# Optimization experiments

Hardware: AMD Instinct MI355X
Metric: run time of the kernel (lower is better)

Reference implementation:

```python
import jax, jax.numpy as jnp
import numpy as np

NUM_USER, NUM_ITEM, NUM_TIME = 200000, 100000, 5000
P, Q, R = 32, 32, 32
N = 131072


def _xavier(key, shape):
    fan_in, fan_out = shape[0], int(np.prod(shape[1:]))
    limit = float(np.sqrt(6.0 / (fan_in + fan_out)))
    return jax.random.uniform(key, shape, dtype=jnp.float32, minval=-limit, maxval=limit)


def setup_inputs() -> dict:
    key = jax.random.key(0)
    k1, k2, k3, k4, k5, k6, k7 = jax.random.split(key, 7)
    return {
        "i_input": jax.random.randint(k1, (N,), 0, NUM_USER),
        "j_input": jax.random.randint(k2, (N,), 0, NUM_ITEM),
        "k_input": jax.random.randint(k3, (N,), 0, NUM_TIME),
        "user_embeddings": _xavier(k4, (NUM_USER, P)),
        "item_embeddings": _xavier(k5, (NUM_ITEM, Q)),
        "time_embeddings": _xavier(k6, (NUM_TIME, R)),
        "core_tensor": _xavier(k7, (P, Q, R)),
    }


def reference(i_input, j_input, k_input, user_embeddings, item_embeddings,
              time_embeddings, core_tensor):
    # Gather per-sample embeddings: [n,p], [n,q], [n,r]
    i_embeds = user_embeddings[i_input]
    j_embeds = item_embeddings[j_input]
    k_embeds = time_embeddings[k_input]
    # Fused Tucker contraction: never materialize the (n,p,q,r) outer product.
    # Mathematically identical to einsum('np,nq,nr,pqr->n', ...).
    t = jnp.einsum('np,pqr->nqr', i_embeds, core_tensor)  # [n,q,r]
    t = jnp.einsum('nqr,nq->nr', t, j_embeds)             # [n,r]
    return jnp.einsum('nr,nr->n', t, k_embeds)            # [n]
```

## Files before the change

### kernel.cpp

```cpp
#include <hip/hip_runtime.h>


#define BIN_CAP 128

__device__ __forceinline__ void build_H_body(const float* __restrict__ G,
                                             const float* __restrict__ W,
                                             float* __restrict__ H,
                                             int num_time, int bblk) {
    const int pq4 = threadIdx.x;
    const int kbase = bblk * 8;

    float acc[8][4];
#pragma unroll
    for (int kk = 0; kk < 8; ++kk)
#pragma unroll
        for (int i = 0; i < 4; ++i) acc[kk][i] = 0.f;

#pragma unroll
    for (int r4 = 0; r4 < 8; ++r4) {
        float4 g[4];
#pragma unroll
        for (int i = 0; i < 4; ++i)
            g[i] = *(const float4*)(G + (size_t)(pq4 * 4 + i) * 32 + r4 * 4);
#pragma unroll
        for (int kk = 0; kk < 8; ++kk) {
            int k = kbase + kk;
            int kc = (k < num_time) ? k : (num_time - 1);
            float4 w = *(const float4*)(W + (size_t)kc * 32 + r4 * 4);
#pragma unroll
            for (int i = 0; i < 4; ++i)
                acc[kk][i] += g[i].x * w.x + g[i].y * w.y + g[i].z * w.z + g[i].w * w.w;
        }
    }

#pragma unroll
    for (int kk = 0; kk < 8; ++kk) {
        int k = kbase + kk;
        if (k < num_time) {
            float4 o = make_float4(acc[kk][0], acc[kk][1], acc[kk][2], acc[kk][3]);
            *(float4*)(H + (size_t)k * 1024 + pq4 * 4) = o;
        }
    }
}

__device__ __forceinline__ void scatter_body(const int* __restrict__ K,
                                             const int* __restrict__ I,
                                             const int* __restrict__ J,
                                             int* __restrict__ counts,
                                             int4* __restrict__ bins,
                                             int* __restrict__ ovf_cnt,
                                             int4* __restrict__ ovf,
                                             int n, int sblk, int nsblk) {
    for (int idx = sblk * 256 + (int)threadIdx.x; idx < n; idx += nsblk * 256) {
        int k = K[idx];
        int4 rec = make_int4(idx, I[idx], J[idx], k);
        int pos = atomicAdd(&counts[k], 1);
        if (pos < BIN_CAP) {
            bins[(size_t)k * BIN_CAP + pos] = rec;
        } else {
            int o = atomicAdd(ovf_cnt, 1);
            ovf[o] = rec;
        }
    }
}

__global__ __launch_bounds__(256) void fused_prepare(
        const float* __restrict__ G, const float* __restrict__ W,
        float* __restrict__ H,
        const int* __restrict__ K, const int* __restrict__ I,
        const int* __restrict__ J, int* __restrict__ counts,
        int4* __restrict__ bins, int* __restrict__ ovf_cnt,
        int4* __restrict__ ovf, int n, int num_time,
        int nbuild, int nscatter) {
    const int b = blockIdx.x;
    if (b < nbuild) {
        build_H_body(G, W, H, num_time, b);
    } else {
        scatter_body(K, I, J, counts, bins, ovf_cnt, ovf, n, b - nbuild, nscatter);
    }
}

__global__ __launch_bounds__(256) void build_H(const float* __restrict__ G,
                                               const float* __restrict__ W,
                                               float* __restrict__ H,
                                               int num_time) {
    build_H_body(G, W, H, num_time, blockIdx.x);
}

__global__ __launch_bounds__(256) void tucker_eval_grouped(
        const float* __restrict__ U, const float* __restrict__ V,
        const float* __restrict__ H, const int* __restrict__ counts,
        const int4* __restrict__ bins, float* __restrict__ out,
        int num_time, const int* __restrict__ ovf_cnt,
        const int4* __restrict__ ovf) {
    __shared__ float4 Hs4[4][256];
    const int wave = threadIdx.x >> 6;
    const int lane = threadIdx.x & 63;
    const int k = blockIdx.x * 4 + wave;
    const int qq = lane & 7;
    const int s8 = lane >> 3;

    int m = 0;
    if (k < num_time) {
        const float4* __restrict__ Hrow4 = (const float4*)(H + (size_t)k * 1024);
#pragma unroll
        for (int c = 0; c < 4; ++c)
            Hs4[wave][lane + 64 * c] = Hrow4[lane + 64 * c];
        m = counts[k];
        m = (m < BIN_CAP) ? m : BIN_CAP;
    }
    __syncthreads();

    if (k < num_time && m > 0) {
        const int iters = (m + 7) >> 3;
        const float4* __restrict__ Hw = Hs4[wave];
        const int4* __restrict__ bbase = bins + (size_t)k * BIN_CAP;

        int sc = (s8 < m) ? s8 : (m - 1);
        int4 rec = bbase[sc];

        for (int t = 0; t < iters; ++t) {
            const int s = t * 8 + s8;
            const float4* __restrict__ Ur = (const float4*)(U + (size_t)rec.y * 32);
            float4 u[8];
#pragma unroll
            for (int p4 = 0; p4 < 8; ++p4) u[p4] = Ur[p4];
            float4 v4 = ((const float4*)(V + (size_t)rec.z * 32))[qq];

            int sn = s + 8;
            sn = (sn < m) ? sn : (m - 1);
            int4 rec_n = bbase[sn];

            float4 acc = make_float4(0.f, 0.f, 0.f, 0.f);
#pragma unroll
            for (int p4 = 0; p4 < 8; ++p4) {
                float4 h;
                h = Hw[(p4 * 4 + 0) * 8 + qq];
                acc.x += u[p4].x * h.x; acc.y += u[p4].x * h.y;
                acc.z += u[p4].x * h.z; acc.w += u[p4].x * h.w;
                h = Hw[(p4 * 4 + 1) * 8 + qq];
                acc.x += u[p4].y * h.x; acc.y += u[p4].y * h.y;
                acc.z += u[p4].y * h.z; acc.w += u[p4].y * h.w;
                h = Hw[(p4 * 4 + 2) * 8 + qq];
                acc.x += u[p4].z * h.x; acc.y += u[p4].z * h.y;
                acc.z += u[p4].z * h.z; acc.w += u[p4].z * h.w;
                h = Hw[(p4 * 4 + 3) * 8 + qq];
                acc.x += u[p4].w * h.x; acc.y += u[p4].w * h.y;
                acc.z += u[p4].w * h.z; acc.w += u[p4].w * h.w;
            }
            float sd = acc.x * v4.x + acc.y * v4.y + acc.z * v4.z + acc.w * v4.w;
            sd += __shfl_xor(sd, 1, 64);
            sd += __shfl_xor(sd, 2, 64);
            sd += __shfl_xor(sd, 4, 64);
            if (s < m && qq == 0) out[rec.x] = sd;
            rec = rec_n;
        }
    }

    const int cnt = *ovf_cnt;
    if (cnt > 0) {
        const int gwave = (int)blockIdx.x * 4 + wave;
        const int nw = (int)gridDim.x * 4;
        const int pg = lane >> 3;
        for (int s = gwave; s < cnt; s += nw) {
            int4 rec = ovf[s];
            const float4* __restrict__ Hrow = (const float4*)(H + (size_t)rec.w * 1024);
            const float* __restrict__ Ur = U + (size_t)rec.y * 32;

            float4 acc = make_float4(0.f, 0.f, 0.f, 0.f);
#pragma unroll
            for (int it = 0; it < 4; ++it) {
                float4 h = Hrow[lane + it * 64];
                float up = Ur[pg + it * 8];
                acc.x += up * h.x; acc.y += up * h.y;
                acc.z += up * h.z; acc.w += up * h.w;
            }
#pragma unroll
            for (int off = 8; off < 64; off <<= 1) {
                acc.x += __shfl_xor(acc.x, off, 64);
                acc.y += __shfl_xor(acc.y, off, 64);
                acc.z += __shfl_xor(acc.z, off, 64);
                acc.w += __shfl_xor(acc.w, off, 64);
            }
            float4 v4 = ((const float4*)(V + (size_t)rec.z * 32))[qq];
            float sd = acc.x * v4.x + acc.y * v4.y + acc.z * v4.z + acc.w * v4.w;
            sd += __shfl_xor(sd, 1, 64);
            sd += __shfl_xor(sd, 2, 64);
            sd += __shfl_xor(sd, 4, 64);
            if (lane == 0) out[rec.x] = sd;
        }
    }
}

__global__ __launch_bounds__(256) void tucker_eval(const int* __restrict__ I,
                                                   const int* __restrict__ J,
                                                   const int* __restrict__ K,
                                                   const float* __restrict__ U,
                                                   const float* __restrict__ V,
                                                   const float* __restrict__ H,
                                                   float* __restrict__ out,
                                                   int n_samples) {
    const int wave = (int)((blockIdx.x * (unsigned)blockDim.x + threadIdx.x) >> 6);
    const int lane = threadIdx.x & 63;
    if (wave >= n_samples) return;
    const int i = I[wave];
    const int j = J[wave];
    const int k = K[wave];
    const int qq = lane & 7;
    const int pg = lane >> 3;
    const float4* __restrict__ Hrow = (const float4*)(H + (size_t)k * 1024);
    const float* __restrict__ Urow = U + (size_t)i * 32;
    float4 acc = make_float4(0.f, 0.f, 0.f, 0.f);
#pragma unroll
    for (int it = 0; it < 4; ++it) {
        float4 h = Hrow[lane + it * 64];
        float up = Urow[pg + it * 8];
        acc.x += up * h.x; acc.y += up * h.y;
        acc.z += up * h.z; acc.w += up * h.w;
    }
#pragma unroll
    for (int off = 8; off < 64; off <<= 1) {
        acc.x += __shfl_xor(acc.x, off, 64);
        acc.y += __shfl_xor(acc.y, off, 64);
        acc.z += __shfl_xor(acc.z, off, 64);
        acc.w += __shfl_xor(acc.w, off, 64);
    }
    float4 v4 = ((const float4*)(V + (size_t)j * 32))[qq];
    float s = acc.x * v4.x + acc.y * v4.y + acc.z * v4.z + acc.w * v4.w;
    s += __shfl_xor(s, 1, 64);
    s += __shfl_xor(s, 2, 64);
    s += __shfl_xor(s, 4, 64);
    if (lane == 0) out[wave] = s;
}

__global__ __launch_bounds__(256) void tucker_direct(const int* __restrict__ I,
                                                     const int* __restrict__ J,
                                                     const int* __restrict__ K,
                                                     const float* __restrict__ U,
                                                     const float* __restrict__ V,
                                                     const float* __restrict__ W,
                                                     const float* __restrict__ G,
                                                     float* __restrict__ out,
                                                     int n_samples) {
    __shared__ float Gc[4 * 32 * 32];
    const int n = blockIdx.x * blockDim.x + threadIdx.x;
    const bool active = (n < n_samples);
    int i = 0, j = 0, k = 0;
    if (active) { i = I[n]; j = J[n]; k = K[n]; }
    float4 w4[8];
#pragma unroll
    for (int r4 = 0; r4 < 8; ++r4)
        w4[r4] = ((const float4*)(W + (size_t)k * 32))[r4];
    float v[32];
#pragma unroll
    for (int q4 = 0; q4 < 8; ++q4) {
        float4 t = ((const float4*)(V + (size_t)j * 32))[q4];
        v[q4 * 4 + 0] = t.x; v[q4 * 4 + 1] = t.y;
        v[q4 * 4 + 2] = t.z; v[q4 * 4 + 3] = t.w;
    }
    const float* __restrict__ Urow = U + (size_t)i * 32;
    float acc = 0.f;
    for (int c = 0; c < 8; ++c) {
        __syncthreads();
#pragma unroll
        for (int t = 0; t < 4; ++t) {
            int idx = threadIdx.x + t * 256;
            ((float4*)Gc)[idx] = ((const float4*)(G + (size_t)c * 4096))[idx];
        }
        __syncthreads();
        for (int pp = 0; pp < 4; ++pp) {
            float up = Urow[c * 4 + pp];
#pragma unroll
            for (int q = 0; q < 32; ++q) {
                float t0 = 0.f;
#pragma unroll
                for (int r4 = 0; r4 < 8; ++r4) {
                    float4 g = ((const float4*)Gc)[pp * 256 + q * 8 + r4];
                    t0 += g.x * w4[r4].x + g.y * w4[r4].y + g.z * w4[r4].z + g.w * w4[r4].w;
                }
                acc += up * v[q] * t0;
            }
        }
    }
    if (active) out[n] = acc;
}

extern "C" void kernel_launch(void* const* d_in, const int* in_sizes, int n_in,
                              void* d_out, int out_size, void* d_ws, size_t ws_size,
                              hipStream_t stream) {
    const int*   I = (const int*)d_in[0];
    const int*   J = (const int*)d_in[1];
    const int*   K = (const int*)d_in[2];
    const float* U = (const float*)d_in[3];
    const float* V = (const float*)d_in[4];
    const float* W = (const float*)d_in[5];
    const float* G = (const float*)d_in[6];
    float* out = (float*)d_out;

    const int n_samples = in_sizes[0];
    const int num_time = in_sizes[5] / 32;

    const size_t h_bytes = (size_t)num_time * 1024 * sizeof(float);
    const size_t z_bytes = (size_t)(num_time + 1) * sizeof(int);
    const size_t z_pad = (z_bytes + 15) & ~(size_t)15;
    const size_t bins_bytes = (size_t)num_time * BIN_CAP * sizeof(int4);
    const size_t ovf_bytes = (size_t)n_samples * sizeof(int4);
    const size_t need_full = h_bytes + z_pad + bins_bytes + ovf_bytes;

    if (ws_size >= need_full) {
        float* H       = (float*)d_ws;
        int*   counts  = (int*)((char*)d_ws + h_bytes);
        int*   ovf_cnt = counts + num_time;
        int4*  bins    = (int4*)((char*)d_ws + h_bytes + z_pad);
        int4*  ovf     = (int4*)((char*)d_ws + h_bytes + z_pad + bins_bytes);

        const int nbuild = (num_time + 7) / 8;
        const int nscatter = 512;

        hipMemsetAsync(counts, 0, z_bytes, stream);
        fused_prepare<<<nbuild + nscatter, 256, 0, stream>>>(
            G, W, H, K, I, J, counts, bins, ovf_cnt, ovf,
            n_samples, num_time, nbuild, nscatter);
        tucker_eval_grouped<<<(num_time + 3) / 4, 256, 0, stream>>>(
            U, V, H, counts, bins, out, num_time, ovf_cnt, ovf);
    } else if (ws_size >= h_bytes) {
        float* H = (float*)d_ws;
        build_H<<<(num_time + 7) / 8, 256, 0, stream>>>(G, W, H, num_time);
        const long long total_threads = (long long)n_samples * 64;
        tucker_eval<<<(int)((total_threads + 255) / 256), 256, 0, stream>>>(
            I, J, K, U, V, H, out, n_samples);
    } else {
        tucker_direct<<<(n_samples + 255) / 256, 256, 0, stream>>>(
            I, J, K, U, V, W, G, out, n_samples);
    }
}
```

Measured before the change: 135.5 us.

## Fuse memset, binning, H build and eval into one cooperative kernel

Replaces the memset plus two-kernel pipeline with a single cooperative launch that zeroes counters, bins samples by time index, and then, per time group, builds the H slice directly in shared memory before evaluating the samples in that group. This removes the global H buffer write and read and two launch boundaries. In exchange it adds grid-wide syncs, recomputes H per wave from G with many global loads, and requires the whole grid (about 625 blocks) to be co-resident. If the cooperative launch fails, the old path is used.

```diff
diff --git a/kernel.cpp b/kernel.cpp
--- a/kernel.cpp
+++ b/kernel.cpp
@@ -1,7 +1,165 @@
 #include <hip/hip_runtime.h>
+#include <hip/hip_cooperative_groups.h>
+
+namespace cg = cooperative_groups;
 
 
 #define BIN_CAP 128
+
+__global__ __launch_bounds__(256, 4) void tucker_fused_coop(
+        const int* __restrict__ I, const int* __restrict__ J,
+        const int* __restrict__ K,
+        const float* __restrict__ U, const float* __restrict__ V,
+        const float* __restrict__ W, const float* __restrict__ G,
+        int* __restrict__ counts, int4* __restrict__ bins,
+        int* __restrict__ ovf_cnt, int4* __restrict__ ovf,
+        float* __restrict__ out, int n, int num_time, int ngroups) {
+    __shared__ float4 Hs4[4][256];
+    cg::grid_group grid = cg::this_grid();
+
+    const int tid = (int)(blockIdx.x * 256 + threadIdx.x);
+    const int nthr = (int)(gridDim.x * 256);
+
+    for (int c = tid; c < num_time; c += nthr) counts[c] = 0;
+    if (tid == 0) *ovf_cnt = 0;
+    grid.sync();
+
+    for (int idx = tid; idx < n; idx += nthr) {
+        int k = K[idx];
+        int4 rec = make_int4(idx, I[idx], J[idx], k);
+        int pos = atomicAdd(&counts[k], 1);
+        if (pos < BIN_CAP) {
+            bins[(size_t)k * BIN_CAP + pos] = rec;
+        } else {
+            int o = atomicAdd(ovf_cnt, 1);
+            ovf[o] = rec;
+        }
+    }
+    grid.sync();
+
+    const int wave = threadIdx.x >> 6;
+    const int lane = threadIdx.x & 63;
+    const int qq = lane & 7;
+    const int s8 = lane >> 3;
+    const float4* __restrict__ Hw = Hs4[wave];
+
+    for (int gidx = (int)blockIdx.x; gidx < ngroups; gidx += (int)gridDim.x) {
+        __syncthreads();
+        const int k = gidx * 4 + wave;
+        int m = 0;
+        if (k < num_time) {
+            float4 wk[8];
+            const float4* __restrict__ Wr = (const float4*)(W + (size_t)k * 32);
+#pragma unroll
+            for (int r4 = 0; r4 < 8; ++r4) wk[r4] = Wr[r4];
+#pragma unroll
+            for (int t = 0; t < 4; ++t) {
+                const int f = lane + 64 * t;
+                float4 o;
+#pragma unroll
+                for (int e = 0; e < 4; ++e) {
+                    const float4* __restrict__ Gr =
+                        (const float4*)(G + (size_t)(4 * f + e) * 32);
+                    float a = 0.f;
+#pragma unroll
+                    for (int r4 = 0; r4 < 8; ++r4) {
+                        float4 g = Gr[r4];
+                        a += g.x * wk[r4].x + g.y * wk[r4].y +
+                             g.z * wk[r4].z + g.w * wk[r4].w;
+                    }
+                    if (e == 0) o.x = a;
+                    else if (e == 1) o.y = a;
+                    else if (e == 2) o.z = a;
+                    else o.w = a;
+                }
+                Hs4[wave][f] = o;
+            }
+            m = counts[k];
+            m = (m < BIN_CAP) ? m : BIN_CAP;
+        }
+
+        if (k < num_time && m > 0) {
+            const int iters = (m + 7) >> 3;
+            const int4* __restrict__ bbase = bins + (size_t)k * BIN_CAP;
+
+            int sc = (s8 < m) ? s8 : (m - 1);
+            int4 rec = bbase[sc];
+
+            for (int t = 0; t < iters; ++t) {
+                const int s = t * 8 + s8;
+                const float4* __restrict__ Ur =
+                    (const float4*)(U + (size_t)rec.y * 32);
+                float4 u[8];
+#pragma unroll
+                for (int p4 = 0; p4 < 8; ++p4) u[p4] = Ur[p4];
+                float4 v4 = ((const float4*)(V + (size_t)rec.z * 32))[qq];
+
+                int sn = s + 8;
+                sn = (sn < m) ? sn : (m - 1);
+                int4 rec_n = bbase[sn];
+
+                float4 acc = make_float4(0.f, 0.f, 0.f, 0.f);
+#pragma unroll
+                for (int p4 = 0; p4 < 8; ++p4) {
+                    float4 h;
+                    h = Hw[(p4 * 4 + 0) * 8 + qq];
+                    acc.x += u[p4].x * h.x; acc.y += u[p4].x * h.y;
+                    acc.z += u[p4].x * h.z; acc.w += u[p4].x * h.w;
+                    h = Hw[(p4 * 4 + 1) * 8 + qq];
+                    acc.x += u[p4].y * h.x; acc.y += u[p4].y * h.y;
+                    acc.z += u[p4].y * h.z; acc.w += u[p4].y * h.w;
+                    h = Hw[(p4 * 4 + 2) * 8 + qq];
+                    acc.x += u[p4].z * h.x; acc.y += u[p4].z * h.y;
+                    acc.z += u[p4].z * h.z; acc.w += u[p4].z * h.w;
+                    h = Hw[(p4 * 4 + 3) * 8 + qq];
+                    acc.x += u[p4].w * h.x; acc.y += u[p4].w * h.y;
+                    acc.z += u[p4].w * h.z; acc.w += u[p4].w * h.w;
+                }
+                float sd = acc.x * v4.x + acc.y * v4.y + acc.z * v4.z + acc.w * v4.w;
+                sd += __shfl_xor(sd, 1, 64);
+                sd += __shfl_xor(sd, 2, 64);
+                sd += __shfl_xor(sd, 4, 64);
+                if (s < m && qq == 0) out[rec.x] = sd;
+                rec = rec_n;
+            }
+        }
+
+        if (k < num_time) {
+            const int cnt = *ovf_cnt;
+            if (cnt > 0) {
+                const int pg = lane >> 3;
+                for (int s = 0; s < cnt; ++s) {
+                    int4 rec = ovf[s];
+                    if (rec.w != k) continue;
+                    const float* __restrict__ Ur2 = U + (size_t)rec.y * 32;
+                    float4 acc = make_float4(0.f, 0.f, 0.f, 0.f);
+#pragma unroll
+                    for (int it = 0; it < 4; ++it) {
+                        float4 h = Hw[lane + it * 64];
+                        float up = Ur2[pg + it * 8];
+                        acc.x += up * h.x; acc.y += up * h.y;
+                        acc.z += up * h.z; acc.w += up * h.w;
+                    }
+#pragma unroll
+                    for (int off = 8; off < 64; off <<= 1) {
+                        acc.x += __shfl_xor(acc.x, off, 64);
+                        acc.y += __shfl_xor(acc.y, off, 64);
+                        acc.z += __shfl_xor(acc.z, off, 64);
+                        acc.w += __shfl_xor(acc.w, off, 64);
+                    }
+                    float4 v4 = ((const float4*)(V + (size_t)rec.z * 32))[qq];
+                    float sd = acc.x * v4.x + acc.y * v4.y +
+                               acc.z * v4.z + acc.w * v4.w;
+                    sd += __shfl_xor(sd, 1, 64);
+                    sd += __shfl_xor(sd, 2, 64);
+                    sd += __shfl_xor(sd, 4, 64);
+                    if (lane == 0) out[rec.x] = sd;
+                }
+            }
+        }
+    }
+}
+
 
 __device__ __forceinline__ void build_H_body(const float* __restrict__ G,
                                              const float* __restrict__ W,
@@ -314,9 +472,24 @@
         int4*  bins    = (int4*)((char*)d_ws + h_bytes + z_pad);
         int4*  ovf     = (int4*)((char*)d_ws + h_bytes + z_pad + bins_bytes);
 
+        const int ngroups = (num_time + 3) / 4;
+        int grid = (ngroups + 1) / 2;
+        if (grid < 1) grid = 1;
+
+        int n_arg = n_samples, nt_arg = num_time, ng_arg = ngroups;
+        void* args[] = {
+            (void*)&I, (void*)&J, (void*)&K,
+            (void*)&U, (void*)&V, (void*)&W, (void*)&G,
+            (void*)&counts, (void*)&bins, (void*)&ovf_cnt, (void*)&ovf,
+            (void*)&out, (void*)&n_arg, (void*)&nt_arg, (void*)&ng_arg,
+        };
+        hipError_t err = hipLaunchCooperativeKernel(
+            (const void*)tucker_fused_coop, dim3(grid), dim3(256), args, 0, stream);
+        if (err == hipSuccess) return;
+        (void)hipGetLastError();
+
         const int nbuild = (num_time + 7) / 8;
         const int nscatter = 512;
-
         hipMemsetAsync(counts, 0, z_bytes, stream);
         fused_prepare<<<nbuild + nscatter, 256, 0, stream>>>(
             G, W, H, K, I, J, counts, bins, ovf_cnt, ovf,
```

After: 385.8 us. 185% more time.

## Assign one block per time bin and stage bin records in shared memory

Applied to the files above, without the earlier changes.

The grouped evaluation kernel now launches one 256-thread block per time index instead of one wave per time index. All four waves share a single H row in LDS, and the bin records are preloaded into shared memory, so each pass covers 32 samples rather than 8. The aim is fewer serial iterations per bin and better latency hiding across the gathers of U and V. In exchange it launches four times as many blocks, drops the explicit next-record prefetch, and leaves threads idle when a bin holds few samples (about 26 on average here).

```diff
diff --git a/kernel.cpp b/kernel.cpp
--- a/kernel.cpp
+++ b/kernel.cpp
@@ -87,64 +87,51 @@
     build_H_body(G, W, H, num_time, blockIdx.x);
 }
 
-__global__ __launch_bounds__(256) void tucker_eval_grouped(
+__global__ __launch_bounds__(256) void tucker_eval_bpk(
         const float* __restrict__ U, const float* __restrict__ V,
         const float* __restrict__ H, const int* __restrict__ counts,
         const int4* __restrict__ bins, float* __restrict__ out,
         int num_time, const int* __restrict__ ovf_cnt,
         const int4* __restrict__ ovf) {
-    __shared__ float4 Hs4[4][256];
-    const int wave = threadIdx.x >> 6;
-    const int lane = threadIdx.x & 63;
-    const int k = blockIdx.x * 4 + wave;
-    const int qq = lane & 7;
-    const int s8 = lane >> 3;
-
-    int m = 0;
-    if (k < num_time) {
-        const float4* __restrict__ Hrow4 = (const float4*)(H + (size_t)k * 1024);
-#pragma unroll
-        for (int c = 0; c < 4; ++c)
-            Hs4[wave][lane + 64 * c] = Hrow4[lane + 64 * c];
-        m = counts[k];
-        m = (m < BIN_CAP) ? m : BIN_CAP;
-    }
+    __shared__ float4 Hs[256];
+    __shared__ int4 Rs[BIN_CAP];
+    const int tid = threadIdx.x;
+    const int k = (int)blockIdx.x;
+    const int qq = tid & 7;
+    const int g = tid >> 3;
+
+    int m = counts[k];
+    m = (m < BIN_CAP) ? m : BIN_CAP;
+
+    const float4* __restrict__ Hrow = (const float4*)(H + (size_t)k * 1024);
+    Hs[tid] = Hrow[tid];
+    if (tid < m) Rs[tid] = bins[(size_t)k * BIN_CAP + tid];
     __syncthreads();
 
-    if (k < num_time && m > 0) {
-        const int iters = (m + 7) >> 3;
-        const float4* __restrict__ Hw = Hs4[wave];
-        const int4* __restrict__ bbase = bins + (size_t)k * BIN_CAP;
-
-        int sc = (s8 < m) ? s8 : (m - 1);
-        int4 rec = bbase[sc];
-
-        for (int t = 0; t < iters; ++t) {
-            const int s = t * 8 + s8;
+    for (int s0 = 0; s0 < m; s0 += 32) {
+        const int s = s0 + g;
+        if (s < m) {
+            int4 rec = Rs[s];
             const float4* __restrict__ Ur = (const float4*)(U + (size_t)rec.y * 32);
             float4 u[8];
 #pragma unroll
             for (int p4 = 0; p4 < 8; ++p4) u[p4] = Ur[p4];
             float4 v4 = ((const float4*)(V + (size_t)rec.z * 32))[qq];
 
-            int sn = s + 8;
-            sn = (sn < m) ? sn : (m - 1);
-            int4 rec_n = bbase[sn];
-
             float4 acc = make_float4(0.f, 0.f, 0.f, 0.f);
 #pragma unroll
             for (int p4 = 0; p4 < 8; ++p4) {
                 float4 h;
-                h = Hw[(p4 * 4 + 0) * 8 + qq];
+                h = Hs[(p4 * 4 + 0) * 8 + qq];
                 acc.x += u[p4].x * h.x; acc.y += u[p4].x * h.y;
                 acc.z += u[p4].x * h.z; acc.w += u[p4].x * h.w;
-                h = Hw[(p4 * 4 + 1) * 8 + qq];
+                h = Hs[(p4 * 4 + 1) * 8 + qq];
                 acc.x += u[p4].y * h.x; acc.y += u[p4].y * h.y;
                 acc.z += u[p4].y * h.z; acc.w += u[p4].y * h.w;
-                h = Hw[(p4 * 4 + 2) * 8 + qq];
+                h = Hs[(p4 * 4 + 2) * 8 + qq];
                 acc.x += u[p4].z * h.x; acc.y += u[p4].z * h.y;
                 acc.z += u[p4].z * h.z; acc.w += u[p4].z * h.w;
-                h = Hw[(p4 * 4 + 3) * 8 + qq];
+                h = Hs[(p4 * 4 + 3) * 8 + qq];
                 acc.x += u[p4].w * h.x; acc.y += u[p4].w * h.y;
                 acc.z += u[p4].w * h.z; acc.w += u[p4].w * h.w;
             }
@@ -152,25 +139,27 @@
             sd += __shfl_xor(sd, 1, 64);
             sd += __shfl_xor(sd, 2, 64);
             sd += __shfl_xor(sd, 4, 64);
-            if (s < m && qq == 0) out[rec.x] = sd;
-            rec = rec_n;
+            if (qq == 0) out[rec.x] = sd;
         }
     }
 
     const int cnt = *ovf_cnt;
     if (cnt > 0) {
-        const int gwave = (int)blockIdx.x * 4 + wave;
+        const int wave = tid >> 6;
+        const int lane = tid & 63;
+        const int gwave = k * 4 + wave;
         const int nw = (int)gridDim.x * 4;
         const int pg = lane >> 3;
+        const int qq6 = lane & 7;
         for (int s = gwave; s < cnt; s += nw) {
             int4 rec = ovf[s];
-            const float4* __restrict__ Hrow = (const float4*)(H + (size_t)rec.w * 1024);
+            const float4* __restrict__ Hrow2 = (const float4*)(H + (size_t)rec.w * 1024);
             const float* __restrict__ Ur = U + (size_t)rec.y * 32;
 
             float4 acc = make_float4(0.f, 0.f, 0.f, 0.f);
 #pragma unroll
             for (int it = 0; it < 4; ++it) {
-                float4 h = Hrow[lane + it * 64];
+                float4 h = Hrow2[lane + it * 64];
                 float up = Ur[pg + it * 8];
                 acc.x += up * h.x; acc.y += up * h.y;
                 acc.z += up * h.z; acc.w += up * h.w;
@@ -182,7 +171,7 @@
                 acc.z += __shfl_xor(acc.z, off, 64);
                 acc.w += __shfl_xor(acc.w, off, 64);
             }
-            float4 v4 = ((const float4*)(V + (size_t)rec.z * 32))[qq];
+            float4 v4 = ((const float4*)(V + (size_t)rec.z * 32))[qq6];
             float sd = acc.x * v4.x + acc.y * v4.y + acc.z * v4.z + acc.w * v4.w;
             sd += __shfl_xor(sd, 1, 64);
             sd += __shfl_xor(sd, 2, 64);
@@ -321,7 +310,7 @@
         fused_prepare<<<nbuild + nscatter, 256, 0, stream>>>(
             G, W, H, K, I, J, counts, bins, ovf_cnt, ovf,
             n_samples, num_time, nbuild, nscatter);
-        tucker_eval_grouped<<<(num_time + 3) / 4, 256, 0, stream>>>(
+        tucker_eval_bpk<<<num_time, 256, 0, stream>>>(
             U, V, H, counts, bins, out, num_time, ovf_cnt, ovf);
     } else if (ws_size >= h_bytes) {
         float* H = (float*)d_ws;
```

After: 126.1 us. -6.9%, faster.
